# Performance work log

Hardware: AMD Instinct MI355X
Metric: run time of the kernel (lower is better)

## Reference

```python
import jax, jax.numpy as jnp
from jax import lax
import numpy as np

NX = 512
LENGTH = 0.1
BCS = [[[0.025, 0.0], [0.075, 0.0]]]
BATCH = 32
COF = 0.25 * (LENGTH / (NX - 1)) ** 2  # 0.25 * stride^2 / temper_coefficient


def _make_mask():
    # Dirichlet boundary mask G (1 in interior, 0 on bc segments), per torch logic
    G = np.ones((1, 1, NX, NX), dtype=np.float32)
    for bc in BCS:
        if bc[0][1] == 0 and bc[1][1] == 0:
            i0 = round(bc[0][0] * NX / LENGTH); i1 = round(bc[1][0] * NX / LENGTH)
            G[..., i0:i1, :1] = 0.0
        elif bc[0][1] == LENGTH and bc[1][1] == LENGTH:
            i0 = round(bc[0][0] * NX / LENGTH); i1 = round(bc[1][0] * NX / LENGTH)
            G[..., i0:i1, -1:] = 0.0
        elif bc[0][0] == 0 and bc[1][0] == 0:
            i0 = round(bc[0][1] * NX / LENGTH); i1 = round(bc[1][1] * NX / LENGTH)
            G[..., :1, i0:i1] = 0.0
        elif bc[0][0] == LENGTH and bc[1][0] == LENGTH:
            i0 = round(bc[0][1] * NX / LENGTH); i1 = round(bc[1][1] * NX / LENGTH)
            G[..., -1:, i0:i1] = 0.0
        else:
            raise ValueError('bc error!')
    return jnp.asarray(G)

G_MASK = _make_mask()


def setup_inputs() -> dict:
    key = jax.random.key(0)
    k1, k2 = jax.random.split(key)
    layout = jax.random.normal(k1, (BATCH, 1, NX, NX), dtype=jnp.float32)
    heat = jax.random.normal(k2, (BATCH, 1, NX, NX), dtype=jnp.float32)
    return {"layout": layout, "heat": heat, "n_iter": 20}


def reference(layout, heat, n_iter):
    f = COF * layout  # source term
    G = G_MASK

    def step(x, _):
        # reflect-pad then 5-point (cross) stencil average == conv2d with the
        # [[0,.25,0],[.25,0,.25],[0,.25,0]] kernel
        p = jnp.pad(x, ((0, 0), (0, 0), (1, 1), (1, 1)), mode='reflect')
        jac = 0.25 * (p[..., :-2, 1:-1] + p[..., 2:, 1:-1]
                      + p[..., 1:-1, :-2] + p[..., 1:-1, 2:])
        return G * (jac + f), None

    # first torch iteration pads heat*G; subsequent iterations pad x (already masked)
    x, _ = lax.scan(step, heat * G, None, length=n_iter)
    return x
```

## Files before the change

### kernel.cpp

```cpp
#include <hip/hip_runtime.h>


constexpr int NXc = 512;
constexpr int QC  = 128;
constexpr int Rr  = 32;
constexpr int NBR = NXc / Rr;
constexpr int NB  = NBR * 32;
constexpr int GRP = 8;
constexpr int MR0 = 128;
constexpr int MR1 = 384;

template <int KK, int VMAXK, bool FIRST>
__global__ __launch_bounds__(1024)
void jacobi_reg(const float* __restrict__ src, const float* __restrict__ lay,
                float* __restrict__ dst, float cof)
{
    constexpr int HALFK = VMAXK / GRP;
    __shared__ float4 rowbuf[2][14][QC];
    __shared__ float  scal[2][GRP][HALFK][2];

    const int tid    = threadIdx.x;
    const int c4     = tid & (QC - 1);
    const int grp    = tid >> 7;
    const int vstart = grp * HALFK;

    const int band = blockIdx.x;
    const int bi   = band >> 4;
    const int br   = band & (NBR - 1);
    const int r0   = br * Rr;
    const bool top = (br == 0), bot = (br == NBR - 1);
    const int H0   = top ? 0 : KK;
    const int V    = H0 + Rr + (bot ? 0 : KK);
    const int v0g  = r0 - H0;
    const size_t base = (size_t)bi * NXc * QC;
    const float4* __restrict__ srcq = reinterpret_cast<const float4*>(src) + base;
    const float4* __restrict__ layq = reinterpret_cast<const float4*>(lay) + base;
    float4* __restrict__ dstq = reinterpret_cast<float4*>(dst) + base;

    float4 st[HALFK], fr[HALFK];
    #pragma unroll
    for (int j = 0; j < HALFK; ++j) {
        const int v  = vstart + j;
        const int gc = (v < V) ? (v0g + v) : (v0g + V - 1);
        float4 val = srcq[(size_t)gc * QC + c4];
        if (FIRST) {
            if (c4 == 0 && gc >= MR0 && gc < MR1) val.x = 0.f;
        }
        st[j] = val;
        const float4 f = layq[(size_t)gc * QC + c4];
        fr[j] = make_float4(cof * f.x, cof * f.y, cof * f.z, cof * f.w);
    }

    #pragma unroll
    for (int t = 1; t <= KK; ++t) {
        const int par = t & 1;
        if (grp <= GRP - 2) rowbuf[par][grp][c4]     = st[HALFK - 1];
        if (grp >= 1)       rowbuf[par][6 + grp][c4] = st[0];
        if (c4 == 63) {
            #pragma unroll
            for (int j = 0; j < HALFK; ++j) scal[par][grp][j][0] = st[j].w;
        }
        if (c4 == 64) {
            #pragma unroll
            for (int j = 0; j < HALFK; ++j) scal[par][grp][j][1] = st[j].x;
        }
        __syncthreads();

        const float4 upN = (grp >= 1)       ? rowbuf[par][grp - 1][c4] : st[0];
        const float4 dnN = (grp <= GRP - 2) ? rowbuf[par][7 + grp][c4] : st[HALFK - 1];

        float4 prev_old = upN;
        #pragma unroll
        for (int j = 0; j < HALFK; ++j) {
            const int g = v0g + vstart + j;
            const float4 cur = st[j];
            const float4 nxt = (j < HALFK - 1) ? st[j + 1] : dnN;
            const float4 up  = (j > 0) ? prev_old : upN;
            const float4 upe = (g == 0)       ? nxt : up;
            const float4 dne = (g == NXc - 1) ? up  : nxt;

            float lf = __shfl_up(cur.w, 1);
            float rt = __shfl_down(cur.x, 1);
            if (c4 == 0)        lf = cur.y;
            else if (c4 == 64)  lf = scal[par][grp][j][0];
            if (c4 == QC - 1)   rt = cur.z;
            else if (c4 == 63)  rt = scal[par][grp][j][1];

            float4 o;
            o.x = 0.25f * (((upe.x + dne.x) + lf   ) + cur.y) + fr[j].x;
            o.y = 0.25f * (((upe.y + dne.y) + cur.x) + cur.z) + fr[j].y;
            o.z = 0.25f * (((upe.z + dne.z) + cur.y) + cur.w) + fr[j].z;
            o.w = 0.25f * (((upe.w + dne.w) + cur.z) + rt   ) + fr[j].w;
            if (c4 == 0 && g >= MR0 && g < MR1) o.x = 0.f;
            prev_old = cur;
            st[j] = o;
        }
    }

    #pragma unroll
    for (int j = 0; j < HALFK; ++j) {
        const int v = vstart + j;
        if (v >= H0 && v < H0 + Rr) {
            dstq[(size_t)(v0g + v) * QC + c4] = st[j];
        }
    }
}

extern "C" void kernel_launch(void* const* d_in, const int* in_sizes, int n_in,
                              void* d_out, int out_size, void* d_ws, size_t ws_size,
                              hipStream_t stream)
{
    const float* layout = (const float*)d_in[0];
    const float* heat   = (const float*)d_in[1];
    float* out = (float*)d_out;
    float* ws  = (float*)d_ws;

    const float cof = (float)(0.25 * (0.1 / 511.0) * (0.1 / 511.0));

    dim3 grid(NB), block(1024);
    jacobi_reg<12, 32 + 2 * 12, true ><<<grid, block, 0, stream>>>(heat, layout, ws,  cof);
    jacobi_reg< 8, 32 + 2 *  8, false><<<grid, block, 0, stream>>>(ws,   layout, out, cof);
}
```

Measured before the change: 156.3 us.

## Map each row to one wavefront with two float4 per lane and bf16 source

```diff
diff --git a/kernel.cpp b/kernel.cpp
--- a/kernel.cpp
+++ b/kernel.cpp
@@ -10,19 +10,24 @@
 constexpr int MR0 = 128;
 constexpr int MR1 = 384;
 
+__device__ __forceinline__ unsigned pack_bf2(float lo, float hi) {
+    return (__float_as_uint(lo) >> 16) | (__float_as_uint(hi) & 0xFFFF0000u);
+}
+__device__ __forceinline__ float unpk_lo(unsigned p) { return __uint_as_float(p << 16); }
+__device__ __forceinline__ float unpk_hi(unsigned p) { return __uint_as_float(p & 0xFFFF0000u); }
+
 template <int KK, int VMAXK, bool FIRST>
-__global__ __launch_bounds__(1024)
-void jacobi_reg(const float* __restrict__ src, const float* __restrict__ lay,
-                float* __restrict__ dst, float cof)
+__global__ __launch_bounds__(512, 2)
+void jacobi_wave(const float* __restrict__ src, const float* __restrict__ lay,
+                 float* __restrict__ dst, float cof)
 {
     constexpr int HALFK = VMAXK / GRP;
     __shared__ float4 rowbuf[2][14][QC];
-    __shared__ float  scal[2][GRP][HALFK][2];
 
-    const int tid    = threadIdx.x;
-    const int c4     = tid & (QC - 1);
-    const int grp    = tid >> 7;
-    const int vstart = grp * HALFK;
+    const int tid  = threadIdx.x;
+    const int lane = tid & 63;
+    const int w    = tid >> 6;
+    const int vstart = w * HALFK;
 
     const int band = blockIdx.x;
     const int bi   = band >> 4;
@@ -37,63 +42,72 @@
     const float4* __restrict__ layq = reinterpret_cast<const float4*>(lay) + base;
     float4* __restrict__ dstq = reinterpret_cast<float4*>(dst) + base;
 
-    float4 st[HALFK], fr[HALFK];
+    float4 stA[HALFK], stB[HALFK];
+    uint4  frp[HALFK];
     #pragma unroll
     for (int j = 0; j < HALFK; ++j) {
         const int v  = vstart + j;
         const int gc = (v < V) ? (v0g + v) : (v0g + V - 1);
-        float4 val = srcq[(size_t)gc * QC + c4];
+        float4 a = srcq[(size_t)gc * QC + 2 * lane];
+        float4 b = srcq[(size_t)gc * QC + 2 * lane + 1];
         if (FIRST) {
-            if (c4 == 0 && gc >= MR0 && gc < MR1) val.x = 0.f;
+            if (lane == 0 && gc >= MR0 && gc < MR1) a.x = 0.f;
         }
-        st[j] = val;
-        const float4 f = layq[(size_t)gc * QC + c4];
-        fr[j] = make_float4(cof * f.x, cof * f.y, cof * f.z, cof * f.w);
+        stA[j] = a; stB[j] = b;
+        const float4 fa = layq[(size_t)gc * QC + 2 * lane];
+        const float4 fb = layq[(size_t)gc * QC + 2 * lane + 1];
+        frp[j] = make_uint4(pack_bf2(cof * fa.x, cof * fa.y),
+                            pack_bf2(cof * fa.z, cof * fa.w),
+                            pack_bf2(cof * fb.x, cof * fb.y),
+                            pack_bf2(cof * fb.z, cof * fb.w));
     }
 
-    #pragma unroll
+    #pragma unroll 1
     for (int t = 1; t <= KK; ++t) {
         const int par = t & 1;
-        if (grp <= GRP - 2) rowbuf[par][grp][c4]     = st[HALFK - 1];
-        if (grp >= 1)       rowbuf[par][6 + grp][c4] = st[0];
-        if (c4 == 63) {
-            #pragma unroll
-            for (int j = 0; j < HALFK; ++j) scal[par][grp][j][0] = st[j].w;
+        if (w <= GRP - 2) {
+            rowbuf[par][w][lane]      = stA[HALFK - 1];
+            rowbuf[par][w][64 + lane] = stB[HALFK - 1];
         }
-        if (c4 == 64) {
-            #pragma unroll
-            for (int j = 0; j < HALFK; ++j) scal[par][grp][j][1] = st[j].x;
+        if (w >= 1) {
+            rowbuf[par][6 + w][lane]      = stA[0];
+            rowbuf[par][6 + w][64 + lane] = stB[0];
         }
         __syncthreads();
 
-        const float4 upN = (grp >= 1)       ? rowbuf[par][grp - 1][c4] : st[0];
-        const float4 dnN = (grp <= GRP - 2) ? rowbuf[par][7 + grp][c4] : st[HALFK - 1];
+        const float4 upNA = (w >= 1) ? rowbuf[par][w - 1][lane]      : stA[0];
+        const float4 upNB = (w >= 1) ? rowbuf[par][w - 1][64 + lane] : stB[0];
+        const float4 dnNA = (w <= GRP - 2) ? rowbuf[par][7 + w][lane]      : stA[HALFK - 1];
+        const float4 dnNB = (w <= GRP - 2) ? rowbuf[par][7 + w][64 + lane] : stB[HALFK - 1];
 
-        float4 prev_old = upN;
+        float4 prevA = upNA, prevB = upNB;
         #pragma unroll
         for (int j = 0; j < HALFK; ++j) {
             const int g = v0g + vstart + j;
-            const float4 cur = st[j];
-            const float4 nxt = (j < HALFK - 1) ? st[j + 1] : dnN;
-            const float4 up  = (j > 0) ? prev_old : upN;
-            const float4 upe = (g == 0)       ? nxt : up;
-            const float4 dne = (g == NXc - 1) ? up  : nxt;
+            const float4 cA = stA[j], cB = stB[j];
+            const float4 nA = (j < HALFK - 1) ? stA[j + 1] : dnNA;
+            const float4 nB = (j < HALFK - 1) ? stB[j + 1] : dnNB;
+            const float4 uA = (j > 0) ? prevA : upNA;
+            const float4 uB = (j > 0) ? prevB : upNB;
+            const float4 upeA = (g == 0) ? nA : uA,  upeB = (g == 0) ? nB : uB;
+            const float4 dneA = (g == NXc - 1) ? uA : nA, dneB = (g == NXc - 1) ? uB : nB;
+            float lf = __shfl_up(cB.w, 1);
+            float rt = __shfl_down(cA.x, 1);
+            if (lane == 0)  lf = cA.y;
+            if (lane == 63) rt = cB.z;
 
-            float lf = __shfl_up(cur.w, 1);
-            float rt = __shfl_down(cur.x, 1);
-            if (c4 == 0)        lf = cur.y;
-            else if (c4 == 64)  lf = scal[par][grp][j][0];
-            if (c4 == QC - 1)   rt = cur.z;
-            else if (c4 == 63)  rt = scal[par][grp][j][1];
-
-            float4 o;
-            o.x = 0.25f * (((upe.x + dne.x) + lf   ) + cur.y) + fr[j].x;
-            o.y = 0.25f * (((upe.y + dne.y) + cur.x) + cur.z) + fr[j].y;
-            o.z = 0.25f * (((upe.z + dne.z) + cur.y) + cur.w) + fr[j].z;
-            o.w = 0.25f * (((upe.w + dne.w) + cur.z) + rt   ) + fr[j].w;
-            if (c4 == 0 && g >= MR0 && g < MR1) o.x = 0.f;
-            prev_old = cur;
-            st[j] = o;
+            float4 oA, oB;
+            oA.x = 0.25f * ((upeA.x + dneA.x) + (lf   + cA.y)) + unpk_lo(frp[j].x);
+            oA.y = 0.25f * ((upeA.y + dneA.y) + (cA.x + cA.z)) + unpk_hi(frp[j].x);
+            oA.z = 0.25f * ((upeA.z + dneA.z) + (cA.y + cA.w)) + unpk_lo(frp[j].y);
+            oA.w = 0.25f * ((upeA.w + dneA.w) + (cA.z + cB.x)) + unpk_hi(frp[j].y);
+            oB.x = 0.25f * ((upeB.x + dneB.x) + (cA.w + cB.y)) + unpk_lo(frp[j].z);
+            oB.y = 0.25f * ((upeB.y + dneB.y) + (cB.x + cB.z)) + unpk_hi(frp[j].z);
+            oB.z = 0.25f * ((upeB.z + dneB.z) + (cB.y + cB.w)) + unpk_lo(frp[j].w);
+            oB.w = 0.25f * ((upeB.w + dneB.w) + (cB.z + rt  )) + unpk_hi(frp[j].w);
+            if (lane == 0 && g >= MR0 && g < MR1) oA.x = 0.f;
+            prevA = cA; prevB = cB;
+            stA[j] = oA; stB[j] = oB;
         }
     }
 
@@ -101,7 +115,9 @@
     for (int j = 0; j < HALFK; ++j) {
         const int v = vstart + j;
         if (v >= H0 && v < H0 + Rr) {
-            dstq[(size_t)(v0g + v) * QC + c4] = st[j];
+            const int g = v0g + v;
+            dstq[(size_t)g * QC + 2 * lane]     = stA[j];
+            dstq[(size_t)g * QC + 2 * lane + 1] = stB[j];
         }
     }
 }
@@ -117,7 +133,7 @@
 
     const float cof = (float)(0.25 * (0.1 / 511.0) * (0.1 / 511.0));
 
-    dim3 grid(NB), block(1024);
-    jacobi_reg<12, 32 + 2 * 12, true ><<<grid, block, 0, stream>>>(heat, layout, ws,  cof);
-    jacobi_reg< 8, 32 + 2 *  8, false><<<grid, block, 0, stream>>>(ws,   layout, out, cof);
+    dim3 grid(NB), block(512);
+    jacobi_wave<12, 32 + 2 * 12, true ><<<grid, block, 0, stream>>>(heat, layout, ws,  cof);
+    jacobi_wave< 8, 32 + 2 *  8, false><<<grid, block, 0, stream>>>(ws,   layout, out, cof);
 }
```

Result: slower. 163.5 us (+4.6%).
